# Optimization experiments

Measured on AMD Instinct MI355X. Metric: run time of the kernel, lower is better.

## Reference

```python
import jax, jax.numpy as jnp
import numpy as np
from jax import lax


def conv2d(x, w, b=None, pad=0, groups=1):
    y = lax.conv_general_dilated(x, w, (1, 1), [(pad, pad), (pad, pad)],
                                 dimension_numbers=('NCHW', 'OIHW', 'NCHW'),
                                 feature_group_count=groups)
    if b is not None:
        y = y + b[None, :, None, None]
    return y


def prelu(x, a):
    return jnp.where(x > 0, x, a * x)


def box_blur(x, k, p):
    # depthwise uniform box filter, groups=3, 'same' output size
    w = jnp.full((3, 1, k, k), 1.0 / (k * k), x.dtype)
    return conv2d(x, w, pad=p, groups=3)


def head(body, hw, hb, c1, c2):
    h = conv2d(body, hw, hb, pad=1)                      # [B,4,H,W]
    g = jnp.mean(h, axis=(2, 3), keepdims=True)          # CALayer: GAP
    s = jax.nn.sigmoid(conv2d(jax.nn.relu(conv2d(g, c1, pad=0)), c2, pad=0))
    return jax.nn.softmax(h * s, axis=1)                 # Softmax2d over channels


def fuse(x, h):
    # kernel_1 is a 1x1 identity conv -> just x
    m2 = box_blur(x, 5, 2)
    m3 = box_blur(x, 15, 7)
    m4 = box_blur(x, 25, 12)
    return h[:, 0:1] * x + h[:, 1:2] * m2 + h[:, 2:3] * m3 + h[:, 3:4] * m4


def setup_inputs() -> dict:
    key = jax.random.key(0)
    ks = jax.random.split(key, 20)
    f32 = jnp.float32
    d = {}
    d['x'] = jax.random.normal(ks[0], (8, 3, 512, 512), f32)
    # body convs
    d['bw1'] = jax.random.normal(ks[1], (32, 3, 3, 3), f32) * 0.05
    d['bb1'] = jnp.zeros((32,), f32)
    d['a1'] = jnp.full((1,), 0.25, f32)
    d['bw2'] = jax.random.normal(ks[2], (64, 32, 3, 3), f32) * 0.05
    d['bb2'] = jnp.zeros((64,), f32)
    d['a2'] = jnp.full((1,), 0.25, f32)
    d['bw3'] = jax.random.normal(ks[3], (32, 64, 3, 3), f32) * 0.05
    d['bb3'] = jnp.zeros((32,), f32)
    d['a3'] = jnp.full((1,), 0.25, f32)
    for i, k0 in zip((1, 2, 3), (4, 8, 12)):
        d[f'h{i}w'] = jax.random.normal(ks[k0], (4, 32, 3, 3), f32) * 0.05
        d[f'h{i}b'] = jnp.zeros((4,), f32)
        d[f'h{i}c1'] = jax.random.normal(ks[k0 + 1], (4, 4, 1, 1), f32) * 0.1
        d[f'h{i}c2'] = jax.random.normal(ks[k0 + 2], (4, 4, 1, 1), f32) * 0.1
    return d


def reference(x, bw1, bb1, a1, bw2, bb2, a2, bw3, bb3, a3,
              h1w, h1b, h1c1, h1c2,
              h2w, h2b, h2c1, h2c2,
              h3w, h3b, h3c1, h3c2):
    body = prelu(conv2d(x, bw1, bb1, pad=1), a1)
    body = prelu(conv2d(body, bw2, bb2, pad=1), a2)
    body = prelu(conv2d(body, bw3, bb3, pad=1), a3)
    h1 = head(body, h1w, h1b, h1c1, h1c2)
    h2 = head(body, h2w, h2b, h2c1, h2c2)
    h3 = head(body, h3w, h3b, h3c1, h3c2)
    out1 = fuse(x, h1)
    out2 = fuse(out1, h2)
    out3 = fuse(out2, h3)
    return out3
```

## Files before the change

kernel.cpp:

```cpp
#include <hip/hip_runtime.h>
#include <math.h>

#define HWSZ (512*512)

typedef unsigned int u32;
typedef __attribute__((ext_vector_type(8))) short short8;
typedef __attribute__((ext_vector_type(4))) float f32x4;

__device__ __forceinline__ unsigned short f2bf(float f) {
    unsigned u = __float_as_uint(f);
    unsigned r = (u + 0x7FFFu + ((u >> 16) & 1u)) >> 16;
    return (unsigned short)r;
}
__device__ __forceinline__ float bf2f(unsigned short h) {
    return __uint_as_float((unsigned)h << 16);
}
__device__ __forceinline__ u32 packhl(float v) {
    unsigned short h = f2bf(v);
    unsigned short l = f2bf(v - bf2f(h));
    return (u32)h | ((u32)l << 16);
}

#define GRAN  3464
#define APLANE (4 * GRAN)

__global__ void prep_weights(const float* __restrict__ w2, const float* __restrict__ w3,
                             const float* __restrict__ hw1, const float* __restrict__ hw2,
                             const float* __restrict__ hw3,
                             const float* __restrict__ hb1, const float* __restrict__ hb2,
                             const float* __restrict__ hb3,
                             unsigned short* __restrict__ w2h, unsigned short* __restrict__ w2l,
                             unsigned short* __restrict__ w3h, unsigned short* __restrict__ w3l,
                             unsigned short* __restrict__ whh, unsigned short* __restrict__ whl,
                             float* __restrict__ hb16)
{
    int i = blockIdx.x * 256 + threadIdx.x;
    if (i < 18432) {
        int tap = i / 2048, r = i % 2048, co = r / 32, ci = r % 32;
        float v = w2[((co * 32 + ci) * 9) + tap];
        unsigned short h = f2bf(v);
        w2h[i] = h; w2l[i] = f2bf(v - bf2f(h));
    } else if (i < 36864) {
        int e = i - 18432;
        int tap = e / 2048, r = e % 2048, co = r / 64, ci = r % 64;
        float v = w3[((co * 64 + ci) * 9) + tap];
        unsigned short h = f2bf(v);
        w3h[e] = h; w3l[e] = f2bf(v - bf2f(h));
    } else if (i < 41472) {
        int e = i - 36864;
        int tap = e / 512, r = e % 512, co16 = r / 32, ci = r % 32;
        float v = 0.f;
        if (co16 < 12) {
            int hd = co16 >> 2, cl = co16 & 3;
            const float* wp = hd == 0 ? hw1 : (hd == 1 ? hw2 : hw3);
            v = wp[((cl * 32 + ci) * 9) + tap];
        }
        unsigned short h = f2bf(v);
        whh[e] = h; whl[e] = f2bf(v - bf2f(h));
    } else if (i < 41488) {
        int j = i - 41472;
        float v = 0.f;
        if (j < 12) {
            const float* bp = (j >> 2) == 0 ? hb1 : ((j >> 2) == 1 ? hb2 : hb3);
            v = bp[j & 3];
        }
        hb16[j] = v;
    }
}

template<int CIN>
__device__ __forceinline__ void stage_tile(const u32* __restrict__ in,
                                           unsigned short* s_a,
                                           int w, int lane, int x1, int y0, int c0)
{
    const int c16 = lane & 15;
    const int g   = lane >> 4;
    for (int it = w; it < 30; it += 4) {
        int r  = it / 5;
        int cb = it % 5;
        int col = cb * 16 + c16;
        if (col < 66) {
            int gy = y0 - 1 + r;
            int gx = x1 - 1 + col;
            u32 d0=0,d1=0,d2=0,d3=0,d4=0,d5=0,d6=0,d7=0;
            if ((unsigned)gy < 512u && (unsigned)gx < 512u) {
                const uint4* p = (const uint4*)(in + ((size_t)(gy * 512 + gx)) * CIN + c0 + g * 8);
                uint4 A = p[0], B = p[1];
                d0=A.x; d1=A.y; d2=A.z; d3=A.w; d4=B.x; d5=B.y; d6=B.z; d7=B.w;
            }
            uint4 hi, lo;
            hi.x = (d0 & 0xffffu) | (d1 << 16);
            hi.y = (d2 & 0xffffu) | (d3 << 16);
            hi.z = (d4 & 0xffffu) | (d5 << 16);
            hi.w = (d6 & 0xffffu) | (d7 << 16);
            lo.x = (d0 >> 16) | (d1 & 0xffff0000u);
            lo.y = (d2 >> 16) | (d3 & 0xffff0000u);
            lo.z = (d4 >> 16) | (d5 & 0xffff0000u);
            lo.w = (d6 >> 16) | (d7 & 0xffff0000u);
            int e = (r * 72 + col) * 8;
            *(uint4*)(s_a + g * GRAN + e) = hi;
            *(uint4*)(s_a + APLANE + g * GRAN + e) = lo;
        }
    }
}

template<int CIN, int COUT>
__global__ __launch_bounds__(256, 2)
void conv_mfma(const u32* __restrict__ in,
               const unsigned short* __restrict__ wh,
               const unsigned short* __restrict__ wl,
               const float* __restrict__ bias,
               const float* __restrict__ alpha,
               u32* __restrict__ out)
{
    constexpr int NTW = COUT / 16;
    __shared__ __align__(16) unsigned short s_a[2 * APLANE];

    const int tid  = threadIdx.x;
    const int w    = tid >> 6;
    const int lane = tid & 63;
    const int ln   = lane & 15;
    const int quad = lane >> 4;
    const int x1   = blockIdx.x * 64;
    const int y0   = blockIdx.y * 4;

    f32x4 acc[4][NTW];
    #pragma unroll
    for (int mt = 0; mt < 4; ++mt)
        #pragma unroll
        for (int nt = 0; nt < NTW; ++nt)
            acc[mt][nt] = (f32x4){0.f, 0.f, 0.f, 0.f};

    for (int c0 = 0; c0 < CIN; c0 += 32) {
        if (c0) __syncthreads();
        stage_tile<CIN>(in, s_a, w, lane, x1, y0, c0);
        __syncthreads();

        #pragma unroll
        for (int tap = 0; tap < 9; ++tap) {
            const int dy = tap / 3, dx = tap % 3;
            short8 bh[NTW], bl[NTW];
            #pragma unroll
            for (int nt = 0; nt < NTW; ++nt) {
                size_t off = ((size_t)(tap * COUT + nt * 16 + ln)) * CIN + c0 + quad * 8;
                bh[nt] = *(const short8*)(wh + off);
                bl[nt] = *(const short8*)(wl + off);
            }
            short8 ah[4], al[4];
            #pragma unroll
            for (int mt = 0; mt < 4; ++mt) {
                const int mti = w * 4 + mt;
                const int rr  = (mti >> 2) + dy;
                const int col = ((mti & 3) << 4) + ln + dx;
                const int off = quad * GRAN + (rr * 72 + col) * 8;
                ah[mt] = *(const short8*)(s_a + off);
                al[mt] = *(const short8*)(s_a + APLANE + off);
            }
            #pragma unroll
            for (int mt = 0; mt < 4; ++mt)
                #pragma unroll
                for (int nt = 0; nt < NTW; ++nt)
                    acc[mt][nt] = __builtin_amdgcn_mfma_f32_16x16x32_bf16(ah[mt], bh[nt], acc[mt][nt], 0, 0, 0);
            #pragma unroll
            for (int mt = 0; mt < 4; ++mt)
                #pragma unroll
                for (int nt = 0; nt < NTW; ++nt)
                    acc[mt][nt] = __builtin_amdgcn_mfma_f32_16x16x32_bf16(al[mt], bh[nt], acc[mt][nt], 0, 0, 0);
            #pragma unroll
            for (int mt = 0; mt < 4; ++mt)
                #pragma unroll
                for (int nt = 0; nt < NTW; ++nt)
                    acc[mt][nt] = __builtin_amdgcn_mfma_f32_16x16x32_bf16(ah[mt], bl[nt], acc[mt][nt], 0, 0, 0);
        }
    }

    const float av = alpha[0];
    float bs[NTW];
    #pragma unroll
    for (int nt = 0; nt < NTW; ++nt) bs[nt] = bias[nt * 16 + ln];
    #pragma unroll
    for (int mt = 0; mt < 4; ++mt) {
        const int mti = w * 4 + mt;
        const int y   = y0 + (mti >> 2);
        const int xb  = x1 + ((mti & 3) << 4) + quad * 4;
        #pragma unroll
        for (int nt = 0; nt < NTW; ++nt) {
            const int co = nt * 16 + ln;
            #pragma unroll
            for (int reg = 0; reg < 4; ++reg) {
                float t = acc[mt][nt][reg] + bs[nt];
                t = t > 0.f ? t : av * t;
                out[((size_t)(y * 512 + xb + reg)) * COUT + co] = packhl(t);
            }
        }
    }
}

__global__ __launch_bounds__(256, 2)
void head_mfma(const u32* __restrict__ in,
               const unsigned short* __restrict__ wh,
               const unsigned short* __restrict__ wl,
               const float* __restrict__ hb,
               float* __restrict__ h, float* __restrict__ g2, int b)
{
    __shared__ __align__(16) unsigned short s_a[2 * APLANE];
    __shared__ float s_red[4][16];

    const int tid  = threadIdx.x;
    const int w    = tid >> 6;
    const int lane = tid & 63;
    const int ln   = lane & 15;
    const int quad = lane >> 4;
    const int x1   = blockIdx.x * 64;
    const int y0   = blockIdx.y * 4;

    f32x4 acc[4];
    #pragma unroll
    for (int mt = 0; mt < 4; ++mt) acc[mt] = (f32x4){0.f, 0.f, 0.f, 0.f};

    stage_tile<32>(in, s_a, w, lane, x1, y0, 0);
    __syncthreads();

    #pragma unroll
    for (int tap = 0; tap < 9; ++tap) {
        const int dy = tap / 3, dx = tap % 3;
        size_t boff = (size_t)tap * 512 + ln * 32 + quad * 8;
        short8 bh = *(const short8*)(wh + boff);
        short8 bl = *(const short8*)(wl + boff);
        short8 ah[4], al[4];
        #pragma unroll
        for (int mt = 0; mt < 4; ++mt) {
            const int mti = w * 4 + mt;
            const int rr  = (mti >> 2) + dy;
            const int col = ((mti & 3) << 4) + ln + dx;
            const int off = quad * GRAN + (rr * 72 + col) * 8;
            ah[mt] = *(const short8*)(s_a + off);
            al[mt] = *(const short8*)(s_a + APLANE + off);
        }
        #pragma unroll
        for (int mt = 0; mt < 4; ++mt)
            acc[mt] = __builtin_amdgcn_mfma_f32_16x16x32_bf16(ah[mt], bh, acc[mt], 0, 0, 0);
        #pragma unroll
        for (int mt = 0; mt < 4; ++mt)
            acc[mt] = __builtin_amdgcn_mfma_f32_16x16x32_bf16(al[mt], bh, acc[mt], 0, 0, 0);
        #pragma unroll
        for (int mt = 0; mt < 4; ++mt)
            acc[mt] = __builtin_amdgcn_mfma_f32_16x16x32_bf16(ah[mt], bl, acc[mt], 0, 0, 0);
    }

    __syncthreads();
    float* s_h = (float*)s_a;
    const float bs = hb[ln];
    float psum = 0.f;
    #pragma unroll
    for (int mt = 0; mt < 4; ++mt) {
        const int mti  = w * 4 + mt;
        const int base = (mti >> 2) * 64 + ((mti & 3) << 4) + quad * 4;
        #pragma unroll
        for (int reg = 0; reg < 4; ++reg) {
            float v = acc[mt][reg] + bs;
            if (ln < 12) s_h[ln * 260 + base + reg] = v;
            psum += v;
        }
    }
    psum += __shfl_down(psum, 16);
    psum += __shfl_down(psum, 32);
    if (lane < 16) s_red[w][lane] = psum;
    __syncthreads();

    if (tid < 192) {
        const int co = tid >> 4, ch = tid & 15;
        const float* src = s_h + co * 260 + ch * 16;
        float4 v0 = *(const float4*)(src);
        float4 v1 = *(const float4*)(src + 4);
        float4 v2 = *(const float4*)(src + 8);
        float4 v3 = *(const float4*)(src + 12);
        const int hd = co >> 2, cl = co & 3;
        float* dst = h + ((size_t)((hd * 8 + b) * 4 + cl)) * HWSZ
                       + (size_t)(y0 + (ch >> 2)) * 512 + x1 + ((ch & 3) << 4);
        *(float4*)(dst)      = v0;
        *(float4*)(dst + 4)  = v1;
        *(float4*)(dst + 8)  = v2;
        *(float4*)(dst + 12) = v3;
    }
    if (tid < 12) {
        float t = s_red[0][tid] + s_red[1][tid] + s_red[2][tid] + s_red[3][tid];
        atomicAdd(&g2[(tid >> 2) * 32 + b * 4 + (tid & 3)], t);
    }
}

__global__ __launch_bounds__(256)
void conv1_nhwc(const float* __restrict__ x, const float* __restrict__ wgt,
                const float* __restrict__ bias, const float* __restrict__ alpha,
                u32* __restrict__ out)
{
    __shared__ float s_in[3][6][72];
    __shared__ float s_w[3][9][32];
    __shared__ float s_b[32];
    const int tid = threadIdx.x;
    const int x1 = blockIdx.x * 64, y0 = blockIdx.y * 4;

    for (int i = tid; i < 3 * 6 * 66; i += 256) {
        int ci = i / 396, rm = i % 396;
        int r = rm / 66, cc = rm % 66;
        int gy = y0 - 1 + r, gx = x1 - 1 + cc;
        float v = 0.f;
        if ((unsigned)gy < 512u && (unsigned)gx < 512u)
            v = x[(size_t)ci * HWSZ + gy * 512 + gx];
        s_in[ci][r][cc] = v;
    }
    for (int i = tid; i < 864; i += 256) {
        int co = i & 31, rm = i >> 5;
        int ci = rm / 9, tap = rm % 9;
        s_w[ci][tap][co] = wgt[(co * 3 + ci) * 9 + tap];
    }
    if (tid < 32) s_b[tid] = bias[tid];
    __syncthreads();

    const int ty = tid >> 6, tx = tid & 63;
    float acc[32];
    #pragma unroll
    for (int i = 0; i < 32; ++i) acc[i] = 0.f;
    #pragma unroll
    for (int ci = 0; ci < 3; ++ci)
        #pragma unroll
        for (int tap = 0; tap < 9; ++tap) {
            const int dy = tap / 3, dx = tap % 3;
            float iv = s_in[ci][ty + dy][tx + dx];
            #pragma unroll
            for (int c4 = 0; c4 < 8; ++c4) {
                float4 wv = *(const float4*)&s_w[ci][tap][c4 * 4];
                acc[c4*4+0] = fmaf(iv, wv.x, acc[c4*4+0]);
                acc[c4*4+1] = fmaf(iv, wv.y, acc[c4*4+1]);
                acc[c4*4+2] = fmaf(iv, wv.z, acc[c4*4+2]);
                acc[c4*4+3] = fmaf(iv, wv.w, acc[c4*4+3]);
            }
        }
    const float av = alpha[0];
    u32* o = out + ((size_t)((y0 + ty) * 512 + x1 + tx)) * 32;
    #pragma unroll
    for (int c4 = 0; c4 < 8; ++c4) {
        uint4 pk;
        float t;
        t = acc[c4*4+0] + s_b[c4*4+0]; t = t > 0.f ? t : av * t; pk.x = packhl(t);
        t = acc[c4*4+1] + s_b[c4*4+1]; t = t > 0.f ? t : av * t; pk.y = packhl(t);
        t = acc[c4*4+2] + s_b[c4*4+2]; t = t > 0.f ? t : av * t; pk.z = packhl(t);
        t = acc[c4*4+3] + s_b[c4*4+3]; t = t > 0.f ? t : av * t; pk.w = packhl(t);
        *(uint4*)(o + c4 * 4) = pk;
    }
}

__global__ void zero_k(float* p, int n)
{
    int i = blockIdx.x * 256 + threadIdx.x;
    if (i < n) p[i] = 0.f;
}

__global__ void ca_kernel(const float* __restrict__ g,
                          const float* __restrict__ c11, const float* __restrict__ c12,
                          const float* __restrict__ c21, const float* __restrict__ c22,
                          const float* __restrict__ c31, const float* __restrict__ c32,
                          float* __restrict__ sOut)
{
    int t = threadIdx.x;
    if (t >= 24) return;
    int head = t / 8, b = t % 8;
    const float* c1 = head == 0 ? c11 : (head == 1 ? c21 : c31);
    const float* c2 = head == 0 ? c12 : (head == 1 ? c22 : c32);
    float m[4], v[4];
    #pragma unroll
    for (int i = 0; i < 4; ++i) m[i] = g[head * 32 + b * 4 + i] * (1.0f / 262144.0f);
    #pragma unroll
    for (int j = 0; j < 4; ++j) {
        float xv = c1[j*4+0]*m[0] + c1[j*4+1]*m[1] + c1[j*4+2]*m[2] + c1[j*4+3]*m[3];
        v[j] = fmaxf(xv, 0.f);
    }
    #pragma unroll
    for (int j = 0; j < 4; ++j) {
        float xv = c2[j*4+0]*v[0] + c2[j*4+1]*v[1] + c2[j*4+2]*v[2] + c2[j*4+3]*v[3];
        sOut[head * 32 + b * 4 + j] = 1.f / (1.f + __expf(-xv));
    }
}

__global__ __launch_bounds__(256)
void sat_row(const float* __restrict__ src, float* __restrict__ S)
{
    const int y  = blockIdx.x;
    const int bc = blockIdx.y;
    float* Sp = S + (size_t)bc * 263169;
    const int tid = threadIdx.x;
    if (y == 0) {
        for (int i = tid; i < 513; i += 256) Sp[i] = 0.f;
        return;
    }
    const float2* row2 = (const float2*)(src + (size_t)bc * HWSZ + (size_t)(y - 1) * 512);
    float2 ab = row2[tid];
    float ps = ab.x + ab.y;
    float v = ps;
    const int lane = tid & 63;
    #pragma unroll
    for (int off = 1; off < 64; off <<= 1) {
        float u = __shfl_up(v, off);
        if (lane >= off) v += u;
    }
    __shared__ float wsum[4];
    const int wv = tid >> 6;
    if (lane == 63) wsum[wv] = v;
    __syncthreads();
    float woff = 0.f;
    #pragma unroll
    for (int k = 0; k < 4; ++k) if (k < wv) woff += wsum[k];
    float excl = woff + v - ps;
    float* o = Sp + (size_t)y * 513;
    if (tid == 0) o[0] = 0.f;
    o[1 + 2 * tid] = excl + ab.x;
    o[2 + 2 * tid] = excl + ab.x + ab.y;
}

__global__ __launch_bounds__(256)
void sat_col(float* __restrict__ S)
{
    const int bc = blockIdx.x;
    const int c  = 1 + blockIdx.y * 256 + threadIdx.x;
    float* P = S + (size_t)bc * 263169 + c;
    float run = 0.f;
    for (int r0 = 1; r0 <= 512; r0 += 16) {
        float v[16];
        #pragma unroll
        for (int i = 0; i < 16; ++i) v[i] = P[(size_t)(r0 + i) * 513];
        #pragma unroll
        for (int i = 0; i < 16; ++i) { run += v[i]; v[i] = run; }
        #pragma unroll
        for (int i = 0; i < 16; ++i) P[(size_t)(r0 + i) * 513] = v[i];
    }
}

__device__ __forceinline__ float boxsum(const float* __restrict__ S, int y, int x, int p)
{
    int y0 = max(y - p, 0), x0 = max(x - p, 0);
    int y1 = min(y + p, 511) + 1, x1 = min(x + p, 511) + 1;
    return S[y1 * 513 + x1] - S[y0 * 513 + x1] - S[y1 * 513 + x0] + S[y0 * 513 + x0];
}

__global__ __launch_bounds__(256)
void fuse_kernel(const float* __restrict__ cur, const float* __restrict__ h,
                 const float* __restrict__ sv, const float* __restrict__ S,
                 float* __restrict__ out, int head)
{
    const int idx = blockIdx.x * 256 + threadIdx.x;
    const int b   = idx >> 18;
    const int rem = idx & 262143;
    const int y   = rem >> 9;
    const int x   = rem & 511;

    const float* sp = sv + head * 32 + b * 4;
    const float* hp = h + (size_t)((head * 8 + b) * 4) * HWSZ + rem;
    float z0 = hp[0]          * sp[0];
    float z1 = hp[HWSZ]       * sp[1];
    float z2 = hp[2 * HWSZ]   * sp[2];
    float z3 = hp[3 * HWSZ]   * sp[3];
    float m  = fmaxf(fmaxf(z0, z1), fmaxf(z2, z3));
    float e0 = __expf(z0 - m), e1 = __expf(z1 - m), e2 = __expf(z2 - m), e3 = __expf(z3 - m);
    float inv = 1.f / (e0 + e1 + e2 + e3);
    float p0 = e0 * inv, p1 = e1 * inv, p2 = e2 * inv, p3 = e3 * inv;

    #pragma unroll
    for (int c = 0; c < 3; ++c) {
        const float* Sp = S + (size_t)(b * 3 + c) * 263169;
        float xv = cur[((size_t)b * 3 + c) * HWSZ + rem];
        float m2 = boxsum(Sp, y, x, 2)  * (1.f / 25.f);
        float m3 = boxsum(Sp, y, x, 7)  * (1.f / 225.f);
        float m4 = boxsum(Sp, y, x, 12) * (1.f / 625.f);
        out[((size_t)b * 3 + c) * HWSZ + rem] = p0 * xv + p1 * m2 + p2 * m3 + p3 * m4;
    }
}

extern "C" void kernel_launch(void* const* d_in, const int* in_sizes, int n_in,
                              void* d_out, int out_size, void* d_ws, size_t ws_size,
                              hipStream_t stream)
{
    (void)in_sizes; (void)n_in; (void)out_size; (void)ws_size;
    const float* x    = (const float*)d_in[0];
    const float* bw1  = (const float*)d_in[1];
    const float* bb1  = (const float*)d_in[2];
    const float* a1   = (const float*)d_in[3];
    const float* bw2  = (const float*)d_in[4];
    const float* bb2  = (const float*)d_in[5];
    const float* a2   = (const float*)d_in[6];
    const float* bw3  = (const float*)d_in[7];
    const float* bb3  = (const float*)d_in[8];
    const float* a3   = (const float*)d_in[9];
    const float* h1w  = (const float*)d_in[10];
    const float* h1b  = (const float*)d_in[11];
    const float* h1c1 = (const float*)d_in[12];
    const float* h1c2 = (const float*)d_in[13];
    const float* h2w  = (const float*)d_in[14];
    const float* h2b  = (const float*)d_in[15];
    const float* h2c1 = (const float*)d_in[16];
    const float* h2c2 = (const float*)d_in[17];
    const float* h3w  = (const float*)d_in[18];
    const float* h3b  = (const float*)d_in[19];
    const float* h3c1 = (const float*)d_in[20];
    const float* h3c2 = (const float*)d_in[21];

    float* ws   = (float*)d_ws;
    u32*   t1u  = (u32*)ws;
    u32*   t2u  = t1u + 8388608;
    float* hbuf = (float*)(t2u + 16777216);
    float* gbuf = hbuf + 25165824;
    float* sbuf = gbuf + 96;
    unsigned short* wb = (unsigned short*)(sbuf + 96);
    unsigned short* w2h = wb;
    unsigned short* w2l = wb + 18432;
    unsigned short* w3h = wb + 36864;
    unsigned short* w3l = wb + 55296;
    unsigned short* whh = wb + 73728;
    unsigned short* whl = wb + 78336;
    float* hb16 = (float*)(wb + 82944);
    float* SAT  = (float*)t2u;
    float* ping = (float*)t1u;

    dim3 blk(256);

    prep_weights<<<dim3(163), blk, 0, stream>>>(bw2, bw3, h1w, h2w, h3w,
                                                h1b, h2b, h3b,
                                                w2h, w2l, w3h, w3l, whh, whl, hb16);
    zero_k<<<dim3(1), dim3(128), 0, stream>>>(gbuf, 96);

    for (int b = 0; b < 8; ++b) {
        conv1_nhwc<<<dim3(8, 128), blk, 0, stream>>>(x + (size_t)b * 3 * HWSZ,
                                                     bw1, bb1, a1, t1u);
        conv_mfma<32, 64><<<dim3(8, 128), blk, 0, stream>>>(t1u, w2h, w2l, bb2, a2, t2u);
        conv_mfma<64, 32><<<dim3(8, 128), blk, 0, stream>>>(t2u, w3h, w3l, bb3, a3, t1u);
        head_mfma<<<dim3(8, 128), blk, 0, stream>>>(t1u, whh, whl, hb16, hbuf, gbuf, b);
    }

    ca_kernel<<<dim3(1), dim3(64), 0, stream>>>(gbuf, h1c1, h1c2, h2c1, h2c2,
                                                h3c1, h3c2, sbuf);

    const float* cur = x;
    for (int i = 0; i < 3; ++i) {
        sat_row<<<dim3(513, 24), blk, 0, stream>>>(cur, SAT);
        sat_col<<<dim3(24, 2), blk, 0, stream>>>(SAT);
        float* nxt = (i == 2) ? (float*)d_out : ping;
        fuse_kernel<<<dim3(8192), blk, 0, stream>>>(cur, hbuf, sbuf, SAT, nxt, i);
        cur = nxt;
    }
}
```

Measured before the change: 1.430 ms.

## Split activations into hi/lo bf16 planes and load MFMA operands directly from global

Activations are now stored as two separate bf16 planes (hi and lo) instead of interleaved u32 pairs. The conv and head kernels drop their LDS staging and read A operands straight from global memory with per-lane bounds masking. Block indices are also swizzled so consecutive blocks walk down columns. This removes the LDS staging, the repacking and the barriers, but it relies on L1/L2 to absorb the 9x halo re-reads, and the epilogue now writes scattered 2-byte stores.

```diff
diff --git a/kernel.cpp b/kernel.cpp
--- a/kernel.cpp
+++ b/kernel.cpp
@@ -4,47 +4,45 @@
 #define HWSZ (512*512)
 
 typedef unsigned int u32;
+typedef unsigned short u16;
 typedef __attribute__((ext_vector_type(8))) short short8;
 typedef __attribute__((ext_vector_type(4))) float f32x4;
 
-__device__ __forceinline__ unsigned short f2bf(float f) {
+__device__ __forceinline__ u16 f2bf(float f) {
     unsigned u = __float_as_uint(f);
     unsigned r = (u + 0x7FFFu + ((u >> 16) & 1u)) >> 16;
-    return (unsigned short)r;
-}
-__device__ __forceinline__ float bf2f(unsigned short h) {
+    return (u16)r;
+}
+__device__ __forceinline__ float bf2f(u16 h) {
     return __uint_as_float((unsigned)h << 16);
 }
-__device__ __forceinline__ u32 packhl(float v) {
-    unsigned short h = f2bf(v);
-    unsigned short l = f2bf(v - bf2f(h));
-    return (u32)h | ((u32)l << 16);
-}
-
-#define GRAN  3464
-#define APLANE (4 * GRAN)
+
+__device__ __forceinline__ void tile_swizzle(int& xt, int& yt) {
+    xt = (int)blockIdx.y & 7;
+    yt = (int)blockIdx.x * 16 + ((int)blockIdx.y >> 3);
+}
 
 __global__ void prep_weights(const float* __restrict__ w2, const float* __restrict__ w3,
                              const float* __restrict__ hw1, const float* __restrict__ hw2,
                              const float* __restrict__ hw3,
                              const float* __restrict__ hb1, const float* __restrict__ hb2,
                              const float* __restrict__ hb3,
-                             unsigned short* __restrict__ w2h, unsigned short* __restrict__ w2l,
-                             unsigned short* __restrict__ w3h, unsigned short* __restrict__ w3l,
-                             unsigned short* __restrict__ whh, unsigned short* __restrict__ whl,
+                             u16* __restrict__ w2h, u16* __restrict__ w2l,
+                             u16* __restrict__ w3h, u16* __restrict__ w3l,
+                             u16* __restrict__ whh, u16* __restrict__ whl,
                              float* __restrict__ hb16)
 {
     int i = blockIdx.x * 256 + threadIdx.x;
     if (i < 18432) {
         int tap = i / 2048, r = i % 2048, co = r / 32, ci = r % 32;
         float v = w2[((co * 32 + ci) * 9) + tap];
-        unsigned short h = f2bf(v);
+        u16 h = f2bf(v);
         w2h[i] = h; w2l[i] = f2bf(v - bf2f(h));
     } else if (i < 36864) {
         int e = i - 18432;
         int tap = e / 2048, r = e % 2048, co = r / 64, ci = r % 64;
         float v = w3[((co * 64 + ci) * 9) + tap];
-        unsigned short h = f2bf(v);
+        u16 h = f2bf(v);
         w3h[e] = h; w3l[e] = f2bf(v - bf2f(h));
     } else if (i < 41472) {
         int e = i - 36864;
@@ -55,7 +53,7 @@
             const float* wp = hd == 0 ? hw1 : (hd == 1 ? hw2 : hw3);
             v = wp[((cl * 32 + ci) * 9) + tap];
         }
-        unsigned short h = f2bf(v);
+        u16 h = f2bf(v);
         whh[e] = h; whl[e] = f2bf(v - bf2f(h));
     } else if (i < 41488) {
         int j = i - 41472;
@@ -68,61 +66,22 @@
     }
 }
 
-template<int CIN>
-__device__ __forceinline__ void stage_tile(const u32* __restrict__ in,
-                                           unsigned short* s_a,
-                                           int w, int lane, int x1, int y0, int c0)
-{
-    const int c16 = lane & 15;
-    const int g   = lane >> 4;
-    for (int it = w; it < 30; it += 4) {
-        int r  = it / 5;
-        int cb = it % 5;
-        int col = cb * 16 + c16;
-        if (col < 66) {
-            int gy = y0 - 1 + r;
-            int gx = x1 - 1 + col;
-            u32 d0=0,d1=0,d2=0,d3=0,d4=0,d5=0,d6=0,d7=0;
-            if ((unsigned)gy < 512u && (unsigned)gx < 512u) {
-                const uint4* p = (const uint4*)(in + ((size_t)(gy * 512 + gx)) * CIN + c0 + g * 8);
-                uint4 A = p[0], B = p[1];
-                d0=A.x; d1=A.y; d2=A.z; d3=A.w; d4=B.x; d5=B.y; d6=B.z; d7=B.w;
-            }
-            uint4 hi, lo;
-            hi.x = (d0 & 0xffffu) | (d1 << 16);
-            hi.y = (d2 & 0xffffu) | (d3 << 16);
-            hi.z = (d4 & 0xffffu) | (d5 << 16);
-            hi.w = (d6 & 0xffffu) | (d7 << 16);
-            lo.x = (d0 >> 16) | (d1 & 0xffff0000u);
-            lo.y = (d2 >> 16) | (d3 & 0xffff0000u);
-            lo.z = (d4 >> 16) | (d5 & 0xffff0000u);
-            lo.w = (d6 >> 16) | (d7 & 0xffff0000u);
-            int e = (r * 72 + col) * 8;
-            *(uint4*)(s_a + g * GRAN + e) = hi;
-            *(uint4*)(s_a + APLANE + g * GRAN + e) = lo;
-        }
-    }
-}
-
 template<int CIN, int COUT>
-__global__ __launch_bounds__(256, 2)
-void conv_mfma(const u32* __restrict__ in,
-               const unsigned short* __restrict__ wh,
-               const unsigned short* __restrict__ wl,
-               const float* __restrict__ bias,
-               const float* __restrict__ alpha,
-               u32* __restrict__ out)
+__global__ __launch_bounds__(256)
+void conv_mfma(const u16* __restrict__ inh, const u16* __restrict__ inl,
+               const u16* __restrict__ wh, const u16* __restrict__ wl,
+               const float* __restrict__ bias, const float* __restrict__ alpha,
+               u16* __restrict__ outh, u16* __restrict__ outl)
 {
     constexpr int NTW = COUT / 16;
-    __shared__ __align__(16) unsigned short s_a[2 * APLANE];
-
     const int tid  = threadIdx.x;
     const int w    = tid >> 6;
     const int lane = tid & 63;
     const int ln   = lane & 15;
     const int quad = lane >> 4;
-    const int x1   = blockIdx.x * 64;
-    const int y0   = blockIdx.y * 4;
+    int xt, yt; tile_swizzle(xt, yt);
+    const int x1  = xt * 64;
+    const int row = yt * 4 + w;
 
     f32x4 acc[4][NTW];
     #pragma unroll
@@ -131,30 +90,33 @@
         for (int nt = 0; nt < NTW; ++nt)
             acc[mt][nt] = (f32x4){0.f, 0.f, 0.f, 0.f};
 
-    for (int c0 = 0; c0 < CIN; c0 += 32) {
-        if (c0) __syncthreads();
-        stage_tile<CIN>(in, s_a, w, lane, x1, y0, c0);
-        __syncthreads();
-
+    const short8 zz = {0, 0, 0, 0, 0, 0, 0, 0};
+
+    #pragma unroll 1
+    for (int kk = 0; kk < CIN / 32; ++kk) {
         #pragma unroll
         for (int tap = 0; tap < 9; ++tap) {
             const int dy = tap / 3, dx = tap % 3;
+            const int gy = row + dy - 1;
+            const bool rowok = (unsigned)gy < 512u;
+            const int gyc = min(max(gy, 0), 511);
+
             short8 bh[NTW], bl[NTW];
             #pragma unroll
             for (int nt = 0; nt < NTW; ++nt) {
-                size_t off = ((size_t)(tap * COUT + nt * 16 + ln)) * CIN + c0 + quad * 8;
-                bh[nt] = *(const short8*)(wh + off);
-                bl[nt] = *(const short8*)(wl + off);
+                const size_t boff = ((size_t)(tap * COUT + nt * 16 + ln)) * CIN + kk * 32 + quad * 8;
+                bh[nt] = *(const short8*)(wh + boff);
+                bl[nt] = *(const short8*)(wl + boff);
             }
             short8 ah[4], al[4];
             #pragma unroll
             for (int mt = 0; mt < 4; ++mt) {
-                const int mti = w * 4 + mt;
-                const int rr  = (mti >> 2) + dy;
-                const int col = ((mti & 3) << 4) + ln + dx;
-                const int off = quad * GRAN + (rr * 72 + col) * 8;
-                ah[mt] = *(const short8*)(s_a + off);
-                al[mt] = *(const short8*)(s_a + APLANE + off);
+                const int gx  = x1 + mt * 16 + ln + dx - 1;
+                const bool ok = rowok && ((unsigned)gx < 512u);
+                const int gxc = min(max(gx, 0), 511);
+                const size_t off = ((size_t)(gyc * 512 + gxc)) * CIN + kk * 32 + quad * 8;
+                ah[mt] = ok ? *(const short8*)(inh + off) : zz;
+                al[mt] = ok ? *(const short8*)(inl + off) : zz;
             }
             #pragma unroll
             for (int mt = 0; mt < 4; ++mt)
@@ -175,35 +137,34 @@
     }
 
     const float av = alpha[0];
-    float bs[NTW];
-    #pragma unroll
-    for (int nt = 0; nt < NTW; ++nt) bs[nt] = bias[nt * 16 + ln];
-    #pragma unroll
-    for (int mt = 0; mt < 4; ++mt) {
-        const int mti = w * 4 + mt;
-        const int y   = y0 + (mti >> 2);
-        const int xb  = x1 + ((mti & 3) << 4) + quad * 4;
-        #pragma unroll
-        for (int nt = 0; nt < NTW; ++nt) {
-            const int co = nt * 16 + ln;
+    #pragma unroll
+    for (int nt = 0; nt < NTW; ++nt) {
+        const int co = nt * 16 + ln;
+        const float bs = bias[co];
+        #pragma unroll
+        for (int mt = 0; mt < 4; ++mt) {
+            const int px0 = row * 512 + x1 + mt * 16 + quad * 4;
             #pragma unroll
             for (int reg = 0; reg < 4; ++reg) {
-                float t = acc[mt][nt][reg] + bs[nt];
+                float t = acc[mt][nt][reg] + bs;
                 t = t > 0.f ? t : av * t;
-                out[((size_t)(y * 512 + xb + reg)) * COUT + co] = packhl(t);
+                u16 h = f2bf(t);
+                u16 l = f2bf(t - bf2f(h));
+                const size_t o = (size_t)(px0 + reg) * COUT + co;
+                outh[o] = h;
+                outl[o] = l;
             }
         }
     }
 }
 
-__global__ __launch_bounds__(256, 2)
-void head_mfma(const u32* __restrict__ in,
-               const unsigned short* __restrict__ wh,
-               const unsigned short* __restrict__ wl,
+__global__ __launch_bounds__(256)
+void head_mfma(const u16* __restrict__ inh, const u16* __restrict__ inl,
+               const u16* __restrict__ wh, const u16* __restrict__ wl,
                const float* __restrict__ hb,
                float* __restrict__ h, float* __restrict__ g2, int b)
 {
-    __shared__ __align__(16) unsigned short s_a[2 * APLANE];
+    __shared__ float s_h[12 * 260];
     __shared__ float s_red[4][16];
 
     const int tid  = threadIdx.x;
@@ -211,31 +172,34 @@
     const int lane = tid & 63;
     const int ln   = lane & 15;
     const int quad = lane >> 4;
-    const int x1   = blockIdx.x * 64;
-    const int y0   = blockIdx.y * 4;
+    int xt, yt; tile_swizzle(xt, yt);
+    const int x1  = xt * 64;
+    const int y0  = yt * 4;
+    const int row = y0 + w;
 
     f32x4 acc[4];
     #pragma unroll
     for (int mt = 0; mt < 4; ++mt) acc[mt] = (f32x4){0.f, 0.f, 0.f, 0.f};
-
-    stage_tile<32>(in, s_a, w, lane, x1, y0, 0);
-    __syncthreads();
+    const short8 zz = {0, 0, 0, 0, 0, 0, 0, 0};
 
     #pragma unroll
     for (int tap = 0; tap < 9; ++tap) {
         const int dy = tap / 3, dx = tap % 3;
-        size_t boff = (size_t)tap * 512 + ln * 32 + quad * 8;
+        const int gy = row + dy - 1;
+        const bool rowok = (unsigned)gy < 512u;
+        const int gyc = min(max(gy, 0), 511);
+        const size_t boff = (size_t)tap * 512 + ln * 32 + quad * 8;
         short8 bh = *(const short8*)(wh + boff);
         short8 bl = *(const short8*)(wl + boff);
         short8 ah[4], al[4];
         #pragma unroll
         for (int mt = 0; mt < 4; ++mt) {
-            const int mti = w * 4 + mt;
-            const int rr  = (mti >> 2) + dy;
-            const int col = ((mti & 3) << 4) + ln + dx;
-            const int off = quad * GRAN + (rr * 72 + col) * 8;
-            ah[mt] = *(const short8*)(s_a + off);
-            al[mt] = *(const short8*)(s_a + APLANE + off);
+            const int gx  = x1 + mt * 16 + ln + dx - 1;
+            const bool ok = rowok && ((unsigned)gx < 512u);
+            const int gxc = min(max(gx, 0), 511);
+            const size_t off = ((size_t)(gyc * 512 + gxc)) * 32 + quad * 8;
+            ah[mt] = ok ? *(const short8*)(inh + off) : zz;
+            al[mt] = ok ? *(const short8*)(inl + off) : zz;
         }
         #pragma unroll
         for (int mt = 0; mt < 4; ++mt)
@@ -248,14 +212,11 @@
             acc[mt] = __builtin_amdgcn_mfma_f32_16x16x32_bf16(ah[mt], bl, acc[mt], 0, 0, 0);
     }
 
-    __syncthreads();
-    float* s_h = (float*)s_a;
     const float bs = hb[ln];
     float psum = 0.f;
     #pragma unroll
     for (int mt = 0; mt < 4; ++mt) {
-        const int mti  = w * 4 + mt;
-        const int base = (mti >> 2) * 64 + ((mti & 3) << 4) + quad * 4;
+        const int base = w * 64 + mt * 16 + quad * 4;
         #pragma unroll
         for (int reg = 0; reg < 4; ++reg) {
             float v = acc[mt][reg] + bs;
@@ -290,15 +251,16 @@
 }
 
 __global__ __launch_bounds__(256)
-void conv1_nhwc(const float* __restrict__ x, const float* __restrict__ wgt,
-                const float* __restrict__ bias, const float* __restrict__ alpha,
-                u32* __restrict__ out)
+void conv1_split(const float* __restrict__ x, const float* __restrict__ wgt,
+                 const float* __restrict__ bias, const float* __restrict__ alpha,
+                 u16* __restrict__ outh, u16* __restrict__ outl)
 {
     __shared__ float s_in[3][6][72];
     __shared__ float s_w[3][9][32];
     __shared__ float s_b[32];
     const int tid = threadIdx.x;
-    const int x1 = blockIdx.x * 64, y0 = blockIdx.y * 4;
+    int xt, yt; tile_swizzle(xt, yt);
+    const int x1 = xt * 64, y0 = yt * 4;
 
     for (int i = tid; i < 3 * 6 * 66; i += 256) {
         int ci = i / 396, rm = i % 396;
@@ -337,16 +299,22 @@
             }
         }
     const float av = alpha[0];
-    u32* o = out + ((size_t)((y0 + ty) * 512 + x1 + tx)) * 32;
-    #pragma unroll
-    for (int c4 = 0; c4 < 8; ++c4) {
-        uint4 pk;
-        float t;
-        t = acc[c4*4+0] + s_b[c4*4+0]; t = t > 0.f ? t : av * t; pk.x = packhl(t);
-        t = acc[c4*4+1] + s_b[c4*4+1]; t = t > 0.f ? t : av * t; pk.y = packhl(t);
-        t = acc[c4*4+2] + s_b[c4*4+2]; t = t > 0.f ? t : av * t; pk.z = packhl(t);
-        t = acc[c4*4+3] + s_b[c4*4+3]; t = t > 0.f ? t : av * t; pk.w = packhl(t);
-        *(uint4*)(o + c4 * 4) = pk;
+    const size_t px = (size_t)((y0 + ty) * 512 + x1 + tx);
+    u16* oh = outh + px * 32;
+    u16* ol = outl + px * 32;
+    #pragma unroll
+    for (int g = 0; g < 4; ++g) {
+        short8 hv, lv;
+        #pragma unroll
+        for (int k = 0; k < 8; ++k) {
+            float t = acc[g * 8 + k] + s_b[g * 8 + k];
+            t = t > 0.f ? t : av * t;
+            u16 hh = f2bf(t);
+            hv[k] = (short)hh;
+            lv[k] = (short)f2bf(t - bf2f(hh));
+        }
+        *(short8*)(oh + g * 8) = hv;
+        *(short8*)(ol + g * 8) = lv;
     }
 }
 
@@ -504,23 +472,26 @@
     const float* h3c2 = (const float*)d_in[21];
 
     float* ws   = (float*)d_ws;
-    u32*   t1u  = (u32*)ws;
-    u32*   t2u  = t1u + 8388608;
-    float* hbuf = (float*)(t2u + 16777216);
+    u16* t1h = (u16*)ws;
+    u16* t1l = t1h + 8388608;
+    u16* t2h = (u16*)(ws + 8388608);
+    u16* t2l = t2h + 16777216;
+    float* hbuf = ws + 25165824;
     float* gbuf = hbuf + 25165824;
     float* sbuf = gbuf + 96;
-    unsigned short* wb = (unsigned short*)(sbuf + 96);
-    unsigned short* w2h = wb;
-    unsigned short* w2l = wb + 18432;
-    unsigned short* w3h = wb + 36864;
-    unsigned short* w3l = wb + 55296;
-    unsigned short* whh = wb + 73728;
-    unsigned short* whl = wb + 78336;
+    u16* wb  = (u16*)(sbuf + 96);
+    u16* w2h = wb;
+    u16* w2l = wb + 18432;
+    u16* w3h = wb + 36864;
+    u16* w3l = wb + 55296;
+    u16* whh = wb + 73728;
+    u16* whl = wb + 78336;
     float* hb16 = (float*)(wb + 82944);
-    float* SAT  = (float*)t2u;
-    float* ping = (float*)t1u;
+    float* SAT  = ws + 8388608;
+    float* ping = ws;
 
     dim3 blk(256);
+    dim3 cg(8, 128);
 
     prep_weights<<<dim3(163), blk, 0, stream>>>(bw2, bw3, h1w, h2w, h3w,
                                                 h1b, h2b, h3b,
@@ -528,11 +499,11 @@
     zero_k<<<dim3(1), dim3(128), 0, stream>>>(gbuf, 96);
 
     for (int b = 0; b < 8; ++b) {
-        conv1_nhwc<<<dim3(8, 128), blk, 0, stream>>>(x + (size_t)b * 3 * HWSZ,
-                                                     bw1, bb1, a1, t1u);
-        conv_mfma<32, 64><<<dim3(8, 128), blk, 0, stream>>>(t1u, w2h, w2l, bb2, a2, t2u);
-        conv_mfma<64, 32><<<dim3(8, 128), blk, 0, stream>>>(t2u, w3h, w3l, bb3, a3, t1u);
-        head_mfma<<<dim3(8, 128), blk, 0, stream>>>(t1u, whh, whl, hb16, hbuf, gbuf, b);
+        conv1_split<<<cg, blk, 0, stream>>>(x + (size_t)b * 3 * HWSZ,
+                                            bw1, bb1, a1, t1h, t1l);
+        conv_mfma<32, 64><<<cg, blk, 0, stream>>>(t1h, t1l, w2h, w2l, bb2, a2, t2h, t2l);
+        conv_mfma<64, 32><<<cg, blk, 0, stream>>>(t2h, t2l, w3h, w3l, bb3, a3, t1h, t1l);
+        head_mfma<<<cg, blk, 0, stream>>>(t1h, t1l, whh, whl, hb16, hbuf, gbuf, b);
     }
 
     ca_kernel<<<dim3(1), dim3(64), 0, stream>>>(gbuf, h1c1, h1c2, h2c1, h2c2,
```

After: 2.027 ms. +41.7%, slower.
